# Performance work log

Measured on AMD Instinct MI355X. Metric: run time of the kernel, lower is better.

## Reference

```python
import jax, jax.numpy as jnp
import numpy as np

N = 50000      # num nodes
E = 800000     # num edges (avg degree 16)
F_IN = 64      # num_node_features
D = 64         # layer_hidden_dim (= out_channels per layer)
H = 8          # num_heads
C = D // H     # head_dim = 8
L = 5          # num_gnn_layers


def setup_inputs() -> dict:
    key = jax.random.key(0)
    ks = jax.random.split(key, 8)
    x = jax.random.normal(ks[0], (N, F_IN), jnp.float32)
    edge_index = jax.random.randint(ks[1], (2, E), 0, N, dtype=jnp.int32)
    # input embedding Linear(F_IN, D): weight stored as [in, out]
    W_in = jax.random.normal(ks[2], (F_IN, D), jnp.float32) * 0.1
    b_in = jnp.zeros((D,), jnp.float32)
    # per-layer GAT params, stacked over L layers
    lin_w = jax.random.normal(ks[3], (L, D, D), jnp.float32) * 0.1
    lin_b = jnp.zeros((L, D), jnp.float32)
    att = jax.random.normal(ks[4], (L, H, 2 * C), jnp.float32) * 0.1
    out_bias = jnp.zeros((L, D), jnp.float32)
    ln_g = jnp.ones((L, D), jnp.float32)
    ln_b = jnp.zeros((L, D), jnp.float32)
    return {"x": x, "edge_index": edge_index, "W_in": W_in, "b_in": b_in,
            "lin_w": lin_w, "lin_b": lin_b, "att": att, "out_bias": out_bias,
            "ln_g": ln_g, "ln_b": ln_b}


def _gat_layer(h, src, dst, Wl, bl, al, ob, g, b):
    # h: [N, D] -> per-head features [N, H, C]
    hp = (h @ Wl + bl).reshape(N, H, C)
    xi = hp[dst]          # [E, H, C] target-node features (x_i)
    xj = hp[src]          # [E, H, C] source-node features (x_j)
    # cat([x_i, x_j]) . att  == x_i . att[:, :C] + x_j . att[:, C:]
    alpha = jnp.einsum('ehc,hc->eh', xi, al[:, :C]) + \
            jnp.einsum('ehc,hc->eh', xj, al[:, C:])          # [E, H]
    alpha = jax.nn.leaky_relu(alpha, negative_slope=0.2)
    # segment softmax over target index (numerically stable)
    m = jax.ops.segment_max(alpha, dst, num_segments=N)      # [N, H]
    ea = jnp.exp(alpha - m[dst])
    s = jax.ops.segment_sum(ea, dst, num_segments=N)         # [N, H]
    w = ea / (s[dst] + 1e-16)                                # [E, H]
    # message = x_j * alpha, aggr='add'
    agg = jax.ops.segment_sum(xj * w[:, :, None], dst, num_segments=N)  # [N, H, C]
    out = agg.reshape(N, H * C) + ob
    out = jax.nn.elu(out)
    # LayerNorm over feature dim (eval mode: dropout = identity)
    mu = out.mean(-1, keepdims=True)
    var = out.var(-1, keepdims=True)
    return (out - mu) * jax.lax.rsqrt(var + 1e-5) * g + b


def reference(x, edge_index, W_in, b_in, lin_w, lin_b, att, out_bias, ln_g, ln_b):
    src = edge_index[0]
    dst = edge_index[1]   # PyG source_to_target: index = edge_index[1]
    h = jax.nn.relu(x @ W_in + b_in)
    for l in range(L):
        h = _gat_layer(h, src, dst, lin_w[l], lin_b[l], att[l],
                       out_bias[l], ln_g[l], ln_b[l])
    return h
```

## Files before the change

### kernel.cpp

```cpp
#include <hip/hip_runtime.h>
#include <hip/hip_bf16.h>

#define DD 64
#define LL 5
#define KPAD 64
#define L2E 1.4426950408889634f

typedef __attribute__((ext_vector_type(8))) short short8;
typedef __attribute__((ext_vector_type(4))) float float4v;

__device__ __forceinline__ short f2bf_bits(float f) {
    __hip_bfloat16 h = __float2bfloat16(f);
    return *reinterpret_cast<short*>(&h);
}
__device__ __forceinline__ float bfbits2f(short s) {
    __hip_bfloat16 h = *reinterpret_cast<__hip_bfloat16*>(&s);
    return __bfloat162float(h);
}

__device__ __forceinline__ int sniffw(const unsigned short* xb) {
    int lane = threadIdx.x & 63;
    int e = (xb[lane * 2] >> 7) & 0xFF;
    return __any(e >= 134) ? 1 : 0;
}

__global__ void allcvt_k(const void* __restrict__ x, const void* __restrict__ W_in,
                         const void* __restrict__ b_in, const void* __restrict__ lw,
                         const void* __restrict__ lb, const void* __restrict__ att,
                         const void* __restrict__ ob, const void* __restrict__ lg,
                         const void* __restrict__ lbb,
                         unsigned short* __restrict__ xhi, unsigned short* __restrict__ xlo,
                         float* __restrict__ wts,
                         unsigned short* __restrict__ whiT, unsigned short* __restrict__ wloT,
                         int* __restrict__ deg,
                         int nelem, int nxb, int n) {
    int bid = blockIdx.x;
    int fl = sniffw((const unsigned short*)x);
    if (bid < nxb) {
        int i = bid * 256 + threadIdx.x;
        if (i < nelem) {
            float v = fl ? ((const float*)x)[i] : (float)((const __hip_bfloat16*)x)[i];
            short hi = f2bf_bits(v);
            xhi[i] = (unsigned short)hi;
            xlo[i] = (unsigned short)f2bf_bits(v - bfbits2f(hi));
        }
    } else if (bid < nxb + 104) {
        int i = (bid - nxb) * 256 + threadIdx.x;
        if (i >= 26560) return;
        const void* p; int o;
        if      (i < 4096)  { p = W_in; o = i; }
        else if (i < 4160)  { p = b_in; o = i - 4096; }
        else if (i < 24640) { p = lw;   o = i - 4160; }
        else if (i < 24960) { p = lb;   o = i - 24640; }
        else if (i < 25600) { p = att;  o = i - 24960; }
        else if (i < 25920) { p = ob;   o = i - 25600; }
        else if (i < 26240) { p = lg;   o = i - 25920; }
        else                { p = lbb;  o = i - 26240; }
        wts[i] = fl ? ((const float*)p)[o] : (float)((const __hip_bfloat16*)p)[o];
    } else if (bid < nxb + 104 + 96) {
        int i = (bid - nxb - 104) * 256 + threadIdx.x;
        if (i >= 6 * 4096) return;
        const void* p; int o;
        if (i < 4096) { p = W_in; o = i; } else { p = lw; o = i - 4096; }
        float v = fl ? ((const float*)p)[o] : (float)((const __hip_bfloat16*)p)[o];
        short hi = f2bf_bits(v);
        short lo = f2bf_bits(v - bfbits2f(hi));
        int mat = i >> 12, rem = i & 4095, k = rem >> 6, col = rem & 63;
        int t = mat * 4096 + col * 64 + k;
        whiT[t] = (unsigned short)hi;
        wloT[t] = (unsigned short)lo;
    } else {
        int i = (bid - nxb - 104 - 96) * 256 + threadIdx.x;
        if (i < n) deg[i] = 0;
    }
}

__global__ void csrpad_k(const int* __restrict__ src, const int* __restrict__ dst,
                         int* __restrict__ deg, unsigned short* __restrict__ csr_pad,
                         int e, int psize, int n) {
    int p = blockIdx.x & 7;
    int chunk = blockIdx.x >> 3;
    int lo = p * psize;
    int hi = min(lo + psize, n);
    int base = chunk * 2048 + threadIdx.x;
#pragma unroll
    for (int k = 0; k < 8; ++k) {
        int i = base + k * 256;
        if (i < e) {
            int d = dst[i];
            if (d >= lo && d < hi) {
                int slot = atomicAdd(&deg[d], 1);
                if (slot < KPAD) csr_pad[d * KPAD + slot] = (unsigned short)src[i];
            }
        }
    }
}

__device__ __forceinline__ void gemm_from_lds(
        const unsigned short (*AH)[72], const unsigned short (*AL)[72],
        const unsigned short* __restrict__ Whi, const unsigned short* __restrict__ Wlo,
        const float* __restrict__ bias, const float* __restrict__ Att,
        unsigned short* __restrict__ hp_out, float* __restrict__ bd,
        float* __restrict__ ss, int base, int n) {
    int lane = threadIdx.x & 63;
    int wave = threadIdx.x >> 6;
    int m = lane & 15;
    int q = lane >> 4;
    int coln = wave * 16 + m;

    short8 ah0 = *reinterpret_cast<const short8*>(&AH[m][q * 8]);
    short8 ah1 = *reinterpret_cast<const short8*>(&AH[m][32 + q * 8]);
    short8 al0 = *reinterpret_cast<const short8*>(&AL[m][q * 8]);
    short8 al1 = *reinterpret_cast<const short8*>(&AL[m][32 + q * 8]);

    short8 bh0 = *reinterpret_cast<const short8*>(Whi + coln * 64 + q * 8);
    short8 bh1 = *reinterpret_cast<const short8*>(Whi + coln * 64 + 32 + q * 8);
    short8 bl0 = *reinterpret_cast<const short8*>(Wlo + coln * 64 + q * 8);
    short8 bl1 = *reinterpret_cast<const short8*>(Wlo + coln * 64 + 32 + q * 8);

    float4v acc = {0.f, 0.f, 0.f, 0.f};
    acc = __builtin_amdgcn_mfma_f32_16x16x32_bf16(ah0, bh0, acc, 0, 0, 0);
    acc = __builtin_amdgcn_mfma_f32_16x16x32_bf16(al0, bh0, acc, 0, 0, 0);
    acc = __builtin_amdgcn_mfma_f32_16x16x32_bf16(ah0, bl0, acc, 0, 0, 0);
    acc = __builtin_amdgcn_mfma_f32_16x16x32_bf16(ah1, bh1, acc, 0, 0, 0);
    acc = __builtin_amdgcn_mfma_f32_16x16x32_bf16(al1, bh1, acc, 0, 0, 0);
    acc = __builtin_amdgcn_mfma_f32_16x16x32_bf16(ah1, bl1, acc, 0, 0, 0);

    float bc = bias[coln];
    int c_ = m & 7;
    int hh = 2 * wave + (m >> 3);
    float attd = Att[hh * 16 + c_];
    float atts = Att[hh * 16 + 8 + c_];
#pragma unroll
    for (int r = 0; r < 4; ++r) {
        int rr = base + q * 4 + r;
        float v = acc[r] + bc;
        short vb = f2bf_bits(v);
        float vr = bfbits2f(vb);
        if (rr < n) hp_out[(size_t)rr * 64 + coln] = (unsigned short)vb;
        float bdv = vr * attd;
        float ssv = vr * atts;
        bdv += __shfl_xor(bdv, 1, 64);
        bdv += __shfl_xor(bdv, 2, 64);
        bdv += __shfl_xor(bdv, 4, 64);
        ssv += __shfl_xor(ssv, 1, 64);
        ssv += __shfl_xor(ssv, 2, 64);
        ssv += __shfl_xor(ssv, 4, 64);
        if ((m & 7) == 0 && rr < n) {
            bd[rr * 8 + hh] = bdv * L2E;
            ss[rr * 8 + hh] = ssv * L2E;
        }
    }
}

__global__ void __launch_bounds__(256) k0_k(const unsigned short* __restrict__ xhi,
                                            const unsigned short* __restrict__ xlo,
                                            const unsigned short* __restrict__ whiT,
                                            const unsigned short* __restrict__ wloT,
                                            const float* __restrict__ bias_in,
                                            const float* __restrict__ bias_l0,
                                            const float* __restrict__ att0,
                                            unsigned short* __restrict__ hp_out,
                                            float* __restrict__ bd, float* __restrict__ ss,
                                            int n) {
    __shared__ unsigned short AH[16][72];
    __shared__ unsigned short AL[16][72];
    int lane = threadIdx.x & 63;
    int wave = threadIdx.x >> 6;
    int m = lane & 15;
    int q = lane >> 4;
    int coln = wave * 16 + m;
    int base = blockIdx.x * 16;

    {
        int arow = min(base + m, n - 1);
        const unsigned short* ap = xhi + (size_t)arow * 64 + q * 8;
        const unsigned short* alp = xlo + (size_t)arow * 64 + q * 8;
        short8 ah0 = *reinterpret_cast<const short8*>(ap);
        short8 ah1 = *reinterpret_cast<const short8*>(ap + 32);
        short8 al0 = *reinterpret_cast<const short8*>(alp);
        short8 al1 = *reinterpret_cast<const short8*>(alp + 32);
        short8 bh0 = *reinterpret_cast<const short8*>(whiT + coln * 64 + q * 8);
        short8 bh1 = *reinterpret_cast<const short8*>(whiT + coln * 64 + 32 + q * 8);
        short8 bl0 = *reinterpret_cast<const short8*>(wloT + coln * 64 + q * 8);
        short8 bl1 = *reinterpret_cast<const short8*>(wloT + coln * 64 + 32 + q * 8);
        float4v acc = {0.f, 0.f, 0.f, 0.f};
        acc = __builtin_amdgcn_mfma_f32_16x16x32_bf16(ah0, bh0, acc, 0, 0, 0);
        acc = __builtin_amdgcn_mfma_f32_16x16x32_bf16(al0, bh0, acc, 0, 0, 0);
        acc = __builtin_amdgcn_mfma_f32_16x16x32_bf16(ah0, bl0, acc, 0, 0, 0);
        acc = __builtin_amdgcn_mfma_f32_16x16x32_bf16(ah1, bh1, acc, 0, 0, 0);
        acc = __builtin_amdgcn_mfma_f32_16x16x32_bf16(al1, bh1, acc, 0, 0, 0);
        acc = __builtin_amdgcn_mfma_f32_16x16x32_bf16(ah1, bl1, acc, 0, 0, 0);
        float bc = bias_in[coln];
#pragma unroll
        for (int r = 0; r < 4; ++r) {
            float v = fmaxf(acc[r] + bc, 0.f);
            short hi = f2bf_bits(v);
            AH[q * 4 + r][coln] = (unsigned short)hi;
            AL[q * 4 + r][coln] = (unsigned short)f2bf_bits(v - bfbits2f(hi));
        }
    }
    __syncthreads();
    gemm_from_lds(AH, AL, whiT + 4096, wloT + 4096, bias_l0, att0,
                  hp_out, bd, ss, base, n);
}

__global__ void __launch_bounds__(256) layer_k(const unsigned short* __restrict__ hpbf,
                                               const int* __restrict__ deg,
                                               const unsigned short* __restrict__ csr,
                                               const float* __restrict__ bd_in,
                                               const float* __restrict__ ss_in,
                                               const float* __restrict__ ob,
                                               const float* __restrict__ g,
                                               const float* __restrict__ b,
                                               const unsigned short* __restrict__ Wnhi,
                                               const unsigned short* __restrict__ Wnlo,
                                               const float* __restrict__ bias_n,
                                               const float* __restrict__ att_n,
                                               unsigned short* __restrict__ hp_out,
                                               float* __restrict__ bd_out,
                                               float* __restrict__ ss_out,
                                               void* __restrict__ outp,
                                               const unsigned short* __restrict__ xb,
                                               int n, int last) {
    __shared__ unsigned short AH[16][72];
    __shared__ unsigned short AL[16][72];
    int lane = threadIdx.x & 63;
    int wave = threadIdx.x >> 6;
    int base = blockIdx.x * 16;

    int h1 = lane & 7;
    int e1 = lane >> 3;
    int qt = lane >> 4;
    int fq = lane & 15;
    int h2 = fq >> 1;
    int bb = qt * 32 + h2 * 4;

    int fl = last ? sniffw(xb) : 0;

    float r0 = 0.f, r1 = 0.f, r2 = 0.f, r3 = 0.f, rsum = 0.f;

    for (int nd = 0; nd < 4; ++nd) {
        int node = base + wave * 4 + nd;
        if (node < n) {
            int node_u = __builtin_amdgcn_readfirstlane(node);
            float bh1 = bd_in[node_u * 8 + h1];
            int dd = __builtin_amdgcn_readfirstlane(min(deg[node_u], KPAD));
            int nchunk = (dd + 7) >> 3;
            const unsigned short* csrn = csr + node_u * KPAD;
            const unsigned* csrd = (const unsigned*)csrn;

            float s_acc = 0.f;
            float a0 = 0.f, a1 = 0.f, a2 = 0.f, a3 = 0.f;

            int c = 0;
            for (; c + 2 <= nchunk; c += 2) {
                int slotA = c * 8 + e1;
                int slotB = slotA + 8;
                int jA1 = csrn[slotA];
                float aA = bh1 + ss_in[jA1 * 8 + h1];
                aA = (aA > 0.f) ? aA : 0.2f * aA;
                float wA = exp2f(fminf(aA, 60.f));
                float wB = 0.f;
                if (slotB < dd) {
                    int jB1 = csrn[slotB];
                    float aB = bh1 + ss_in[jB1 * 8 + h1];
                    aB = (aB > 0.f) ? aB : 0.2f * aB;
                    wB = exp2f(fminf(aB, 60.f));
                }
                s_acc += wA + wB;
                unsigned sA0 = csrd[c * 4 + 0];
                unsigned sA1 = csrd[c * 4 + 1];
                unsigned sA2 = csrd[c * 4 + 2];
                unsigned sA3 = csrd[c * 4 + 3];
                unsigned sB0 = csrd[c * 4 + 4];
                unsigned sB1 = csrd[c * 4 + 5];
                unsigned sB2 = csrd[c * 4 + 6];
                unsigned sB3 = csrd[c * 4 + 7];
#pragma unroll
                for (int p = 0; p < 2; ++p) {
                    {
                        unsigned dwlo = p ? sA2 : sA0;
                        unsigned dwhi = p ? sA3 : sA1;
                        unsigned dw = (qt & 2) ? dwhi : dwlo;
                        int j = (qt & 1) ? (int)(dw >> 16) : (int)(dw & 0xffffu);
                        j = min(j, n - 1);
                        float we = __int_as_float(
                            __builtin_amdgcn_ds_bpermute(bb + 128 * p, __float_as_int(wA)));
                        uint2 d2 = *reinterpret_cast<const uint2*>(hpbf + (size_t)j * 64 + fq * 4);
                        a0 = fmaf(__int_as_float((int)(d2.x << 16)), we, a0);
                        a1 = fmaf(__int_as_float((int)(d2.x & 0xffff0000u)), we, a1);
                        a2 = fmaf(__int_as_float((int)(d2.y << 16)), we, a2);
                        a3 = fmaf(__int_as_float((int)(d2.y & 0xffff0000u)), we, a3);
                    }
                    {
                        unsigned dwlo = p ? sB2 : sB0;
                        unsigned dwhi = p ? sB3 : sB1;
                        unsigned dw = (qt & 2) ? dwhi : dwlo;
                        int j = (qt & 1) ? (int)(dw >> 16) : (int)(dw & 0xffffu);
                        j = min(j, n - 1);
                        float we = __int_as_float(
                            __builtin_amdgcn_ds_bpermute(bb + 128 * p, __float_as_int(wB)));
                        uint2 d2 = *reinterpret_cast<const uint2*>(hpbf + (size_t)j * 64 + fq * 4);
                        a0 = fmaf(__int_as_float((int)(d2.x << 16)), we, a0);
                        a1 = fmaf(__int_as_float((int)(d2.x & 0xffff0000u)), we, a1);
                        a2 = fmaf(__int_as_float((int)(d2.y << 16)), we, a2);
                        a3 = fmaf(__int_as_float((int)(d2.y & 0xffff0000u)), we, a3);
                    }
                }
            }
            if (c < nchunk) {
                int slot = c * 8 + e1;
                float w = 0.f;
                if (slot < dd) {
                    int j1 = csrn[slot];
                    float a = bh1 + ss_in[j1 * 8 + h1];
                    a = (a > 0.f) ? a : 0.2f * a;
                    w = exp2f(fminf(a, 60.f));
                }
                s_acc += w;
                unsigned s0 = csrd[c * 4 + 0];
                unsigned s1 = csrd[c * 4 + 1];
                unsigned s2 = csrd[c * 4 + 2];
                unsigned s3 = csrd[c * 4 + 3];
#pragma unroll
                for (int p = 0; p < 2; ++p) {
                    unsigned dwlo = p ? s2 : s0;
                    unsigned dwhi = p ? s3 : s1;
                    unsigned dw = (qt & 2) ? dwhi : dwlo;
                    int j = (qt & 1) ? (int)(dw >> 16) : (int)(dw & 0xffffu);
                    j = min(j, n - 1);
                    float we = __int_as_float(
                        __builtin_amdgcn_ds_bpermute(bb + 128 * p, __float_as_int(w)));
                    uint2 d2 = *reinterpret_cast<const uint2*>(hpbf + (size_t)j * 64 + fq * 4);
                    a0 = fmaf(__int_as_float((int)(d2.x << 16)), we, a0);
                    a1 = fmaf(__int_as_float((int)(d2.x & 0xffff0000u)), we, a1);
                    a2 = fmaf(__int_as_float((int)(d2.y << 16)), we, a2);
                    a3 = fmaf(__int_as_float((int)(d2.y & 0xffff0000u)), we, a3);
                }
            }

            float ssum = s_acc;
            ssum += __shfl_xor(ssum, 8, 64);
            ssum += __shfl_xor(ssum, 16, 64);
            ssum += __shfl_xor(ssum, 32, 64);

            a0 += __shfl_xor(a0, 16, 64); a0 += __shfl_xor(a0, 32, 64);
            a1 += __shfl_xor(a1, 16, 64); a1 += __shfl_xor(a1, 32, 64);
            a2 += __shfl_xor(a2, 16, 64); a2 += __shfl_xor(a2, 32, 64);
            a3 += __shfl_xor(a3, 16, 64); a3 += __shfl_xor(a3, 32, 64);

            if (qt == nd) { r0 = a0; r1 = a1; r2 = a2; r3 = a3; rsum = ssum; }
        }
    }

    float sh = __int_as_float(
        __builtin_amdgcn_ds_bpermute((qt * 16 + h2) * 4, __float_as_int(rsum)));
    float rinv = __builtin_amdgcn_rcpf(sh + 1e-16f);
    float4 ob4 = ((const float4*)ob)[fq];
    float o0 = r0 * rinv + ob4.x;
    float o1 = r1 * rinv + ob4.y;
    float o2 = r2 * rinv + ob4.z;
    float o3 = r3 * rinv + ob4.w;
    o0 = (o0 > 0.f) ? o0 : exp2f(o0 * L2E) - 1.f;
    o1 = (o1 > 0.f) ? o1 : exp2f(o1 * L2E) - 1.f;
    o2 = (o2 > 0.f) ? o2 : exp2f(o2 * L2E) - 1.f;
    o3 = (o3 > 0.f) ? o3 : exp2f(o3 * L2E) - 1.f;

    float ps = o0 + o1 + o2 + o3;
#pragma unroll
    for (int d = 1; d < 16; d <<= 1) ps += __shfl_xor(ps, d, 64);
    float mu = ps * (1.f / 64.f);
    float d0 = o0 - mu, d1 = o1 - mu, d2v = o2 - mu, d3 = o3 - mu;
    float sq = d0 * d0 + d1 * d1 + d2v * d2v + d3 * d3;
#pragma unroll
    for (int d = 1; d < 16; d <<= 1) sq += __shfl_xor(sq, d, 64);
    float rstd = __builtin_amdgcn_rsqf(sq * (1.f / 64.f) + 1e-5f);
    float4 g4 = ((const float4*)g)[fq];
    float4 b4 = ((const float4*)b)[fq];
    float y0 = d0 * rstd * g4.x + b4.x;
    float y1 = d1 * rstd * g4.y + b4.y;
    float y2 = d2v * rstd * g4.z + b4.z;
    float y3 = d3 * rstd * g4.w + b4.w;

    int onode = base + wave * 4 + qt;
    if (!last) {
        int ridx = wave * 4 + qt;
        short hb0 = f2bf_bits(y0), hb1 = f2bf_bits(y1);
        short hb2 = f2bf_bits(y2), hb3 = f2bf_bits(y3);
        unsigned hA = (unsigned short)hb0 | ((unsigned)(unsigned short)hb1 << 16);
        unsigned hB = (unsigned short)hb2 | ((unsigned)(unsigned short)hb3 << 16);
        uint2 yh = {hA, hB};
        unsigned lA = (unsigned short)f2bf_bits(y0 - bfbits2f(hb0)) |
                      ((unsigned)(unsigned short)f2bf_bits(y1 - bfbits2f(hb1)) << 16);
        unsigned lB = (unsigned short)f2bf_bits(y2 - bfbits2f(hb2)) |
                      ((unsigned)(unsigned short)f2bf_bits(y3 - bfbits2f(hb3)) << 16);
        uint2 yl = {lA, lB};
        *reinterpret_cast<uint2*>(&AH[ridx][fq * 4]) = yh;
        *reinterpret_cast<uint2*>(&AL[ridx][fq * 4]) = yl;
    } else if (onode < n) {
        if (fl) {
            float4 y = {y0, y1, y2, y3};
            ((float4*)outp)[(size_t)onode * 16 + fq] = y;
        } else {
            unsigned lo = (unsigned short)f2bf_bits(y0) |
                          ((unsigned)(unsigned short)f2bf_bits(y1) << 16);
            unsigned hi = (unsigned short)f2bf_bits(y2) |
                          ((unsigned)(unsigned short)f2bf_bits(y3) << 16);
            uint2 y = {lo, hi};
            ((uint2*)outp)[(size_t)onode * 16 + fq] = y;
        }
    }

    if (last) return;
    __syncthreads();
    gemm_from_lds(AH, AL, Wnhi, Wnlo, bias_n, att_n, hp_out, bd_out, ss_out, base, n);
}

static void* g_pool = nullptr;
static size_t g_pool_sz = 0;

extern "C" void kernel_launch(void* const* d_in, const int* in_sizes, int n_in,
                              void* d_out, int out_size, void* d_ws, size_t ws_size,
                              hipStream_t stream) {
    const void* x    = d_in[0];
    const int* ei    = (const int*)d_in[1];
    const void* W_in = d_in[2];
    const void* b_in = d_in[3];
    const void* lw   = d_in[4];
    const void* lb   = d_in[5];
    const void* att  = d_in[6];
    const void* ob   = d_in[7];
    const void* lg   = d_in[8];
    const void* lbb  = d_in[9];

    const int n = in_sizes[0] / DD;
    const int e = in_sizes[1] / 2;
    const int* src = ei;
    const int* dst = ei + e;

    auto align256 = [](size_t v) { return (v + 255) & ~(size_t)255; };
    size_t need = 0;
    size_t off_xhi  = need; need += align256((size_t)n * DD * 2);
    size_t off_xlo  = need; need += align256((size_t)n * DD * 2);
    size_t off_hpA  = need; need += align256((size_t)n * DD * 2);
    size_t off_hpB  = need; need += align256((size_t)n * DD * 2);
    size_t off_deg  = need; need += align256((size_t)n * 4);
    size_t off_csr  = need; need += align256((size_t)n * KPAD * 2);
    size_t off_wts  = need; need += align256((size_t)26560 * 4);
    size_t off_bdA  = need; need += align256((size_t)n * 8 * 4);
    size_t off_ssA  = need; need += align256((size_t)n * 8 * 4);
    size_t off_bdB  = need; need += align256((size_t)n * 8 * 4);
    size_t off_ssB  = need; need += align256((size_t)n * 8 * 4);
    size_t off_whi  = need; need += align256((size_t)6 * 4096 * 2);
    size_t off_wlo  = need; need += align256((size_t)6 * 4096 * 2);

    char* ws;
    if (ws_size >= need) {
        ws = (char*)d_ws;
    } else {
        if (g_pool == nullptr || g_pool_sz < need) {
            hipMalloc(&g_pool, need);
            g_pool_sz = need;
        }
        ws = (char*)g_pool;
    }

    unsigned short* xhi = (unsigned short*)(ws + off_xhi);
    unsigned short* xlo = (unsigned short*)(ws + off_xlo);
    unsigned short* hpA = (unsigned short*)(ws + off_hpA);
    unsigned short* hpB = (unsigned short*)(ws + off_hpB);
    int* deg     = (int*)(ws + off_deg);
    unsigned short* csr = (unsigned short*)(ws + off_csr);
    float* wts   = (float*)(ws + off_wts);
    float* bdA   = (float*)(ws + off_bdA);
    float* ssA   = (float*)(ws + off_ssA);
    float* bdB   = (float*)(ws + off_bdB);
    float* ssB   = (float*)(ws + off_ssB);
    unsigned short* whiT = (unsigned short*)(ws + off_whi);
    unsigned short* wloT = (unsigned short*)(ws + off_wlo);

    float* wb_in = wts + 4096;
    float* wlb   = wts + 24640;
    float* watt  = wts + 24960;
    float* wob   = wts + 25600;
    float* wlg   = wts + 25920;
    float* wlbb  = wts + 26240;

    int nelem = n * DD;
    int nxb = (nelem + 255) / 256;
    int degb = (n + 255) / 256;
    allcvt_k<<<nxb + 104 + 96 + degb, 256, 0, stream>>>(
        x, W_in, b_in, lw, lb, att, ob, lg, lbb,
        xhi, xlo, wts, whiT, wloT, deg, nelem, nxb, n);

    int psize = (n + 7) / 8;
    int chunks = (e + 2047) / 2048;
    csrpad_k<<<chunks * 8, 256, 0, stream>>>(src, dst, deg, csr, e, psize, n);

    int nb16 = (n + 15) / 16;
    k0_k<<<nb16, 256, 0, stream>>>(xhi, xlo, whiT, wloT, wb_in, wlb, watt,
                                   hpA, bdA, ssA, n);

    for (int l = 0; l < LL; ++l) {
        int last = (l == LL - 1) ? 1 : 0;
        unsigned short* hin = (l & 1) ? hpB : hpA;
        float* bdi = (l & 1) ? bdB : bdA;
        float* ssi = (l & 1) ? ssB : ssA;
        unsigned short* hout = (l & 1) ? hpA : hpB;
        float* bdo = (l & 1) ? bdA : bdB;
        float* sso = (l & 1) ? ssA : ssB;
        layer_k<<<nb16, 256, 0, stream>>>(
            hin, deg, csr, bdi, ssi,
            wob + (size_t)l * DD, wlg + (size_t)l * DD, wlbb + (size_t)l * DD,
            whiT + (size_t)(l + 2) * 4096, wloT + (size_t)(l + 2) * 4096,
            wlb + (size_t)(l + 1) * DD, watt + (size_t)(l + 1) * 128,
            hout, bdo, sso, d_out, (const unsigned short*)x, n, last);
    }
}
```

Measured before the change: 318.7 us.

## Process four nodes per wave concurrently with software-pipelined gathers, 32-row blocks

The per-layer aggregation used to walk a wave's nodes one at a time. It now handles four nodes together in gat_quad, with loads issued ahead of compute in unrolled stages chosen by the maximum chunk count, to raise memory-level parallelism on the neighbor gathers. Each block now covers 32 nodes (8 per wave, in two passes), and the fused next-layer GEMM runs on 32 rows with a new gemm_from_lds32. Buffers are padded so the int4 degree loads and clamped indices stay in range. The cost is higher register pressure, hinted with launch_bounds(256,6), and wasted lanes when the four nodes' degrees differ.

```diff
diff --git a/kernel.cpp b/kernel.cpp
--- a/kernel.cpp
+++ b/kernel.cpp
@@ -16,6 +16,9 @@
 __device__ __forceinline__ float bfbits2f(short s) {
     __hip_bfloat16 h = *reinterpret_cast<__hip_bfloat16*>(&s);
     return __bfloat162float(h);
+}
+__device__ __forceinline__ float bperm(int addr, float v) {
+    return __int_as_float(__builtin_amdgcn_ds_bpermute(addr, __float_as_int(v)));
 }
 
 __device__ __forceinline__ int sniffw(const unsigned short* xb) {
@@ -153,6 +156,67 @@
     }
 }
 
+__device__ __forceinline__ void gemm_from_lds32(
+        const unsigned short (*AH)[72], const unsigned short (*AL)[72],
+        const unsigned short* __restrict__ Whi, const unsigned short* __restrict__ Wlo,
+        const float* __restrict__ bias, const float* __restrict__ Att,
+        unsigned short* __restrict__ hp_out, float* __restrict__ bd,
+        float* __restrict__ ss, int base, int n) {
+    int lane = threadIdx.x & 63;
+    int wave = threadIdx.x >> 6;
+    int m = lane & 15;
+    int q = lane >> 4;
+    int coln = wave * 16 + m;
+
+    short8 bh0 = *reinterpret_cast<const short8*>(Whi + coln * 64 + q * 8);
+    short8 bh1 = *reinterpret_cast<const short8*>(Whi + coln * 64 + 32 + q * 8);
+    short8 bl0 = *reinterpret_cast<const short8*>(Wlo + coln * 64 + q * 8);
+    short8 bl1 = *reinterpret_cast<const short8*>(Wlo + coln * 64 + 32 + q * 8);
+
+    float bc = bias[coln];
+    int c_ = m & 7;
+    int hh = 2 * wave + (m >> 3);
+    float attd = Att[hh * 16 + c_];
+    float atts = Att[hh * 16 + 8 + c_];
+
+#pragma unroll
+    for (int mi = 0; mi < 2; ++mi) {
+        short8 ah0 = *reinterpret_cast<const short8*>(&AH[mi * 16 + m][q * 8]);
+        short8 ah1 = *reinterpret_cast<const short8*>(&AH[mi * 16 + m][32 + q * 8]);
+        short8 al0 = *reinterpret_cast<const short8*>(&AL[mi * 16 + m][q * 8]);
+        short8 al1 = *reinterpret_cast<const short8*>(&AL[mi * 16 + m][32 + q * 8]);
+
+        float4v acc = {0.f, 0.f, 0.f, 0.f};
+        acc = __builtin_amdgcn_mfma_f32_16x16x32_bf16(ah0, bh0, acc, 0, 0, 0);
+        acc = __builtin_amdgcn_mfma_f32_16x16x32_bf16(al0, bh0, acc, 0, 0, 0);
+        acc = __builtin_amdgcn_mfma_f32_16x16x32_bf16(ah0, bl0, acc, 0, 0, 0);
+        acc = __builtin_amdgcn_mfma_f32_16x16x32_bf16(ah1, bh1, acc, 0, 0, 0);
+        acc = __builtin_amdgcn_mfma_f32_16x16x32_bf16(al1, bh1, acc, 0, 0, 0);
+        acc = __builtin_amdgcn_mfma_f32_16x16x32_bf16(ah1, bl1, acc, 0, 0, 0);
+
+#pragma unroll
+        for (int r = 0; r < 4; ++r) {
+            int rr = base + mi * 16 + q * 4 + r;
+            float v = acc[r] + bc;
+            short vb = f2bf_bits(v);
+            float vr = bfbits2f(vb);
+            if (rr < n) hp_out[(size_t)rr * 64 + coln] = (unsigned short)vb;
+            float bdv = vr * attd;
+            float ssv = vr * atts;
+            bdv += __shfl_xor(bdv, 1, 64);
+            bdv += __shfl_xor(bdv, 2, 64);
+            bdv += __shfl_xor(bdv, 4, 64);
+            ssv += __shfl_xor(ssv, 1, 64);
+            ssv += __shfl_xor(ssv, 2, 64);
+            ssv += __shfl_xor(ssv, 4, 64);
+            if ((m & 7) == 0 && rr < n) {
+                bd[rr * 8 + hh] = bdv * L2E;
+                ss[rr * 8 + hh] = ssv * L2E;
+            }
+        }
+    }
+}
+
 __global__ void __launch_bounds__(256) k0_k(const unsigned short* __restrict__ xhi,
                                             const unsigned short* __restrict__ xlo,
                                             const unsigned short* __restrict__ whiT,
@@ -205,7 +269,151 @@
                   hp_out, bd, ss, base, n);
 }
 
-__global__ void __launch_bounds__(256) layer_k(const unsigned short* __restrict__ hpbf,
+#define EXJ(W, j) { unsigned ws_ = (e1 & 4) ? ((e1 & 2) ? W.w : W.z) : ((e1 & 2) ? W.y : W.x); \
+    j = (e1 & 1) ? (int)(ws_ >> 16) : (int)(ws_ & 0xffffu); j = min(j, nm1); }
+#define EXG(W, g0, g1) { unsigned d0_ = (qt & 2) ? W.y : W.x; unsigned d1_ = (qt & 2) ? W.w : W.z; \
+    g0 = (qt & 1) ? (int)(d0_ >> 16) : (int)(d0_ & 0xffffu); \
+    g1 = (qt & 1) ? (int)(d1_ >> 16) : (int)(d1_ & 0xffffu); \
+    g0 = min(g0, nm1); g1 = min(g1, nm1); }
+#define FMA4(V, W, A0, A1, A2, A3) \
+    A0 = fmaf(__int_as_float((int)(V.x << 16)), W, A0); \
+    A1 = fmaf(__int_as_float((int)(V.x & 0xffff0000u)), W, A1); \
+    A2 = fmaf(__int_as_float((int)(V.y << 16)), W, A2); \
+    A3 = fmaf(__int_as_float((int)(V.y & 0xffff0000u)), W, A3);
+
+#define QDECL(ST) uint2 ST##v00, ST##v01, ST##v10, ST##v11, ST##v20, ST##v21, ST##v30, ST##v31; \
+    float ST##ss0, ST##ss1, ST##ss2, ST##ss3;
+
+#define QLOAD(ST, ci) { \
+    uint4 w0_ = c0[ci]; uint4 w1_ = c1[ci]; uint4 w2_ = c2[ci]; uint4 w3_ = c3[ci]; \
+    { int j_; EXJ(w0_, j_) ST##ss0 = ss_in[j_ * 8 + h1]; } \
+    { int j_; EXJ(w1_, j_) ST##ss1 = ss_in[j_ * 8 + h1]; } \
+    { int j_; EXJ(w2_, j_) ST##ss2 = ss_in[j_ * 8 + h1]; } \
+    { int j_; EXJ(w3_, j_) ST##ss3 = ss_in[j_ * 8 + h1]; } \
+    { int g0_, g1_; EXG(w0_, g0_, g1_) \
+      ST##v00 = *reinterpret_cast<const uint2*>(hpbf + (size_t)g0_ * 64 + fq4); \
+      ST##v01 = *reinterpret_cast<const uint2*>(hpbf + (size_t)g1_ * 64 + fq4); } \
+    { int g0_, g1_; EXG(w1_, g0_, g1_) \
+      ST##v10 = *reinterpret_cast<const uint2*>(hpbf + (size_t)g0_ * 64 + fq4); \
+      ST##v11 = *reinterpret_cast<const uint2*>(hpbf + (size_t)g1_ * 64 + fq4); } \
+    { int g0_, g1_; EXG(w2_, g0_, g1_) \
+      ST##v20 = *reinterpret_cast<const uint2*>(hpbf + (size_t)g0_ * 64 + fq4); \
+      ST##v21 = *reinterpret_cast<const uint2*>(hpbf + (size_t)g1_ * 64 + fq4); } \
+    { int g0_, g1_; EXG(w3_, g0_, g1_) \
+      ST##v30 = *reinterpret_cast<const uint2*>(hpbf + (size_t)g0_ * 64 + fq4); \
+      ST##v31 = *reinterpret_cast<const uint2*>(hpbf + (size_t)g1_ * 64 + fq4); } \
+}
+
+#define QCOMP(ST, ci) { \
+    int slot_ = (ci) * 8 + e1; \
+    { float aa_ = bh0 + ST##ss0; aa_ = (aa_ > 0.f) ? aa_ : 0.2f * aa_; \
+      float wg_ = (slot_ < dd0) ? exp2f(fminf(aa_, 60.f)) : 0.f; \
+      s0 += wg_; \
+      float wp0_ = bperm(bb, wg_); float wp1_ = bperm(bb + 128, wg_); \
+      FMA4(ST##v00, wp0_, a00, a01, a02, a03) \
+      FMA4(ST##v01, wp1_, a00, a01, a02, a03) } \
+    { float aa_ = bh1v + ST##ss1; aa_ = (aa_ > 0.f) ? aa_ : 0.2f * aa_; \
+      float wg_ = (slot_ < dd1) ? exp2f(fminf(aa_, 60.f)) : 0.f; \
+      s1 += wg_; \
+      float wp0_ = bperm(bb, wg_); float wp1_ = bperm(bb + 128, wg_); \
+      FMA4(ST##v10, wp0_, a10, a11, a12, a13) \
+      FMA4(ST##v11, wp1_, a10, a11, a12, a13) } \
+    { float aa_ = bh2v + ST##ss2; aa_ = (aa_ > 0.f) ? aa_ : 0.2f * aa_; \
+      float wg_ = (slot_ < dd2) ? exp2f(fminf(aa_, 60.f)) : 0.f; \
+      s2 += wg_; \
+      float wp0_ = bperm(bb, wg_); float wp1_ = bperm(bb + 128, wg_); \
+      FMA4(ST##v20, wp0_, a20, a21, a22, a23) \
+      FMA4(ST##v21, wp1_, a20, a21, a22, a23) } \
+    { float aa_ = bh3v + ST##ss3; aa_ = (aa_ > 0.f) ? aa_ : 0.2f * aa_; \
+      float wg_ = (slot_ < dd3) ? exp2f(fminf(aa_, 60.f)) : 0.f; \
+      s3 += wg_; \
+      float wp0_ = bperm(bb, wg_); float wp1_ = bperm(bb + 128, wg_); \
+      FMA4(ST##v30, wp0_, a30, a31, a32, a33) \
+      FMA4(ST##v31, wp1_, a30, a31, a32, a33) } \
+}
+
+__device__ __forceinline__ void gat_quad(
+        const unsigned short* __restrict__ hpbf,
+        const float* __restrict__ ss_in,
+        const unsigned short* __restrict__ csr,
+        int u0, int u1, int u2, int u3,
+        int dd0, int dd1, int dd2, int dd3,
+        float bh0, float bh1v, float bh2v, float bh3v,
+        int e1, int h1, int qt, int fq4, int bb, int nm1,
+        float& r0, float& r1, float& r2, float& r3, float& rsum) {
+    const uint4* c0 = reinterpret_cast<const uint4*>(csr + (size_t)u0 * KPAD);
+    const uint4* c1 = reinterpret_cast<const uint4*>(csr + (size_t)u1 * KPAD);
+    const uint4* c2 = reinterpret_cast<const uint4*>(csr + (size_t)u2 * KPAD);
+    const uint4* c3 = reinterpret_cast<const uint4*>(csr + (size_t)u3 * KPAD);
+    int ncm = (max(max(dd0, dd1), max(dd2, dd3)) + 7) >> 3;
+
+    float s0 = 0.f, s1 = 0.f, s2 = 0.f, s3 = 0.f;
+    float a00 = 0.f, a01 = 0.f, a02 = 0.f, a03 = 0.f;
+    float a10 = 0.f, a11 = 0.f, a12 = 0.f, a13 = 0.f;
+    float a20 = 0.f, a21 = 0.f, a22 = 0.f, a23 = 0.f;
+    float a30 = 0.f, a31 = 0.f, a32 = 0.f, a33 = 0.f;
+
+    if (ncm <= 2) {
+        QDECL(P) QDECL(Q)
+        QLOAD(P, 0)
+        QLOAD(Q, 1)
+        QCOMP(P, 0)
+        QCOMP(Q, 1)
+    } else if (ncm == 3) {
+        QDECL(P) QDECL(Q) QDECL(R)
+        QLOAD(P, 0)
+        QLOAD(Q, 1)
+        QCOMP(P, 0)
+        QLOAD(R, 2)
+        QCOMP(Q, 1)
+        QCOMP(R, 2)
+    } else if (ncm == 4) {
+        QDECL(P) QDECL(Q) QDECL(R) QDECL(S)
+        QLOAD(P, 0)
+        QLOAD(Q, 1)
+        QCOMP(P, 0)
+        QLOAD(R, 2)
+        QCOMP(Q, 1)
+        QLOAD(S, 3)
+        QCOMP(R, 2)
+        QCOMP(S, 3)
+    } else {
+        for (int c = 0; c < ncm; ++c) {
+            QDECL(T)
+            QLOAD(T, c)
+            QCOMP(T, c)
+        }
+    }
+
+    s0 += __shfl_xor(s0, 8, 64); s0 += __shfl_xor(s0, 16, 64); s0 += __shfl_xor(s0, 32, 64);
+    s1 += __shfl_xor(s1, 8, 64); s1 += __shfl_xor(s1, 16, 64); s1 += __shfl_xor(s1, 32, 64);
+    s2 += __shfl_xor(s2, 8, 64); s2 += __shfl_xor(s2, 16, 64); s2 += __shfl_xor(s2, 32, 64);
+    s3 += __shfl_xor(s3, 8, 64); s3 += __shfl_xor(s3, 16, 64); s3 += __shfl_xor(s3, 32, 64);
+
+    a00 += __shfl_xor(a00, 16, 64); a00 += __shfl_xor(a00, 32, 64);
+    a01 += __shfl_xor(a01, 16, 64); a01 += __shfl_xor(a01, 32, 64);
+    a02 += __shfl_xor(a02, 16, 64); a02 += __shfl_xor(a02, 32, 64);
+    a03 += __shfl_xor(a03, 16, 64); a03 += __shfl_xor(a03, 32, 64);
+    a10 += __shfl_xor(a10, 16, 64); a10 += __shfl_xor(a10, 32, 64);
+    a11 += __shfl_xor(a11, 16, 64); a11 += __shfl_xor(a11, 32, 64);
+    a12 += __shfl_xor(a12, 16, 64); a12 += __shfl_xor(a12, 32, 64);
+    a13 += __shfl_xor(a13, 16, 64); a13 += __shfl_xor(a13, 32, 64);
+    a20 += __shfl_xor(a20, 16, 64); a20 += __shfl_xor(a20, 32, 64);
+    a21 += __shfl_xor(a21, 16, 64); a21 += __shfl_xor(a21, 32, 64);
+    a22 += __shfl_xor(a22, 16, 64); a22 += __shfl_xor(a22, 32, 64);
+    a23 += __shfl_xor(a23, 16, 64); a23 += __shfl_xor(a23, 32, 64);
+    a30 += __shfl_xor(a30, 16, 64); a30 += __shfl_xor(a30, 32, 64);
+    a31 += __shfl_xor(a31, 16, 64); a31 += __shfl_xor(a31, 32, 64);
+    a32 += __shfl_xor(a32, 16, 64); a32 += __shfl_xor(a32, 32, 64);
+    a33 += __shfl_xor(a33, 16, 64); a33 += __shfl_xor(a33, 32, 64);
+
+    if (qt == 0) { r0 = a00; r1 = a01; r2 = a02; r3 = a03; rsum = s0; }
+    if (qt == 1) { r0 = a10; r1 = a11; r2 = a12; r3 = a13; rsum = s1; }
+    if (qt == 2) { r0 = a20; r1 = a21; r2 = a22; r3 = a23; rsum = s2; }
+    if (qt == 3) { r0 = a30; r1 = a31; r2 = a32; r3 = a33; rsum = s3; }
+}
+
+__global__ void __launch_bounds__(256, 6) layer_k(const unsigned short* __restrict__ hpbf,
                                                const int* __restrict__ deg,
                                                const unsigned short* __restrict__ csr,
                                                const float* __restrict__ bd_in,
@@ -223,198 +431,107 @@
                                                void* __restrict__ outp,
                                                const unsigned short* __restrict__ xb,
                                                int n, int last) {
-    __shared__ unsigned short AH[16][72];
-    __shared__ unsigned short AL[16][72];
+    __shared__ unsigned short AH[32][72];
+    __shared__ unsigned short AL[32][72];
     int lane = threadIdx.x & 63;
     int wave = threadIdx.x >> 6;
-    int base = blockIdx.x * 16;
+    int base = blockIdx.x * 32;
 
     int h1 = lane & 7;
     int e1 = lane >> 3;
     int qt = lane >> 4;
     int fq = lane & 15;
+    int fq4 = fq * 4;
     int h2 = fq >> 1;
     int bb = qt * 32 + h2 * 4;
+    int nm1 = n - 1;
 
     int fl = last ? sniffw(xb) : 0;
-
-    float r0 = 0.f, r1 = 0.f, r2 = 0.f, r3 = 0.f, rsum = 0.f;
-
-    for (int nd = 0; nd < 4; ++nd) {
-        int node = base + wave * 4 + nd;
-        if (node < n) {
-            int node_u = __builtin_amdgcn_readfirstlane(node);
-            float bh1 = bd_in[node_u * 8 + h1];
-            int dd = __builtin_amdgcn_readfirstlane(min(deg[node_u], KPAD));
-            int nchunk = (dd + 7) >> 3;
-            const unsigned short* csrn = csr + node_u * KPAD;
-            const unsigned* csrd = (const unsigned*)csrn;
-
-            float s_acc = 0.f;
-            float a0 = 0.f, a1 = 0.f, a2 = 0.f, a3 = 0.f;
-
-            int c = 0;
-            for (; c + 2 <= nchunk; c += 2) {
-                int slotA = c * 8 + e1;
-                int slotB = slotA + 8;
-                int jA1 = csrn[slotA];
-                float aA = bh1 + ss_in[jA1 * 8 + h1];
-                aA = (aA > 0.f) ? aA : 0.2f * aA;
-                float wA = exp2f(fminf(aA, 60.f));
-                float wB = 0.f;
-                if (slotB < dd) {
-                    int jB1 = csrn[slotB];
-                    float aB = bh1 + ss_in[jB1 * 8 + h1];
-                    aB = (aB > 0.f) ? aB : 0.2f * aB;
-                    wB = exp2f(fminf(aB, 60.f));
-                }
-                s_acc += wA + wB;
-                unsigned sA0 = csrd[c * 4 + 0];
-                unsigned sA1 = csrd[c * 4 + 1];
-                unsigned sA2 = csrd[c * 4 + 2];
-                unsigned sA3 = csrd[c * 4 + 3];
-                unsigned sB0 = csrd[c * 4 + 4];
-                unsigned sB1 = csrd[c * 4 + 5];
-                unsigned sB2 = csrd[c * 4 + 6];
-                unsigned sB3 = csrd[c * 4 + 7];
+    int nd0 = base + wave * 8;
+
+#pragma unroll 1
+    for (int pass = 0; pass < 2; ++pass) {
+        int np = nd0 + pass * 4;
+        int4 dv = *reinterpret_cast<const int4*>(deg + np);
+        int dd0 = __builtin_amdgcn_readfirstlane((np + 0 < n) ? min(dv.x, KPAD) : 0);
+        int dd1 = __builtin_amdgcn_readfirstlane((np + 1 < n) ? min(dv.y, KPAD) : 0);
+        int dd2 = __builtin_amdgcn_readfirstlane((np + 2 < n) ? min(dv.z, KPAD) : 0);
+        int dd3 = __builtin_amdgcn_readfirstlane((np + 3 < n) ? min(dv.w, KPAD) : 0);
+        float bh0 = bd_in[min(np + 0, nm1) * 8 + h1];
+        float bh1v = bd_in[min(np + 1, nm1) * 8 + h1];
+        float bh2v = bd_in[min(np + 2, nm1) * 8 + h1];
+        float bh3v = bd_in[min(np + 3, nm1) * 8 + h1];
+        int u0 = __builtin_amdgcn_readfirstlane(min(np + 0, nm1));
+        int u1 = __builtin_amdgcn_readfirstlane(min(np + 1, nm1));
+        int u2 = __builtin_amdgcn_readfirstlane(min(np + 2, nm1));
+        int u3 = __builtin_amdgcn_readfirstlane(min(np + 3, nm1));
+
+        float r0 = 0.f, r1 = 0.f, r2 = 0.f, r3 = 0.f, rsum = 0.f;
+        gat_quad(hpbf, ss_in, csr, u0, u1, u2, u3, dd0, dd1, dd2, dd3,
+                 bh0, bh1v, bh2v, bh3v, e1, h1, qt, fq4, bb, nm1,
+                 r0, r1, r2, r3, rsum);
+
+        float sh = bperm((qt * 16 + h2) * 4, rsum);
+        float rinv = __builtin_amdgcn_rcpf(sh + 1e-16f);
+        float4 ob4 = ((const float4*)ob)[fq];
+        float o0 = r0 * rinv + ob4.x;
+        float o1 = r1 * rinv + ob4.y;
+        float o2 = r2 * rinv + ob4.z;
+        float o3 = r3 * rinv + ob4.w;
+        o0 = (o0 > 0.f) ? o0 : exp2f(o0 * L2E) - 1.f;
+        o1 = (o1 > 0.f) ? o1 : exp2f(o1 * L2E) - 1.f;
+        o2 = (o2 > 0.f) ? o2 : exp2f(o2 * L2E) - 1.f;
+        o3 = (o3 > 0.f) ? o3 : exp2f(o3 * L2E) - 1.f;
+
+        float ps = o0 + o1 + o2 + o3;
 #pragma unroll
-                for (int p = 0; p < 2; ++p) {
-                    {
-                        unsigned dwlo = p ? sA2 : sA0;
-                        unsigned dwhi = p ? sA3 : sA1;
-                        unsigned dw = (qt & 2) ? dwhi : dwlo;
-                        int j = (qt & 1) ? (int)(dw >> 16) : (int)(dw & 0xffffu);
-                        j = min(j, n - 1);
-                        float we = __int_as_float(
-                            __builtin_amdgcn_ds_bpermute(bb + 128 * p, __float_as_int(wA)));
-                        uint2 d2 = *reinterpret_cast<const uint2*>(hpbf + (size_t)j * 64 + fq * 4);
-                        a0 = fmaf(__int_as_float((int)(d2.x << 16)), we, a0);
-                        a1 = fmaf(__int_as_float((int)(d2.x & 0xffff0000u)), we, a1);
-                        a2 = fmaf(__int_as_float((int)(d2.y << 16)), we, a2);
-                        a3 = fmaf(__int_as_float((int)(d2.y & 0xffff0000u)), we, a3);
-                    }
-                    {
-                        unsigned dwlo = p ? sB2 : sB0;
-                        unsigned dwhi = p ? sB3 : sB1;
-                        unsigned dw = (qt & 2) ? dwhi : dwlo;
-                        int j = (qt & 1) ? (int)(dw >> 16) : (int)(dw & 0xffffu);
-                        j = min(j, n - 1);
-                        float we = __int_as_float(
-                            __builtin_amdgcn_ds_bpermute(bb + 128 * p, __float_as_int(wB)));
-                        uint2 d2 = *reinterpret_cast<const uint2*>(hpbf + (size_t)j * 64 + fq * 4);
-                        a0 = fmaf(__int_as_float((int)(d2.x << 16)), we, a0);
-                        a1 = fmaf(__int_as_float((int)(d2.x & 0xffff0000u)), we, a1);
-                        a2 = fmaf(__int_as_float((int)(d2.y << 16)), we, a2);
-                        a3 = fmaf(__int_as_float((int)(d2.y & 0xffff0000u)), we, a3);
-                    }
-                }
+        for (int d = 1; d < 16; d <<= 1) ps += __shfl_xor(ps, d, 64);
+        float mu = ps * (1.f / 64.f);
+        float d0 = o0 - mu, d1 = o1 - mu, d2v = o2 - mu, d3 = o3 - mu;
+        float sq = d0 * d0 + d1 * d1 + d2v * d2v + d3 * d3;
+#pragma unroll
+        for (int d = 1; d < 16; d <<= 1) sq += __shfl_xor(sq, d, 64);
+        float rstd = __builtin_amdgcn_rsqf(sq * (1.f / 64.f) + 1e-5f);
+        float4 g4 = ((const float4*)g)[fq];
+        float4 b4 = ((const float4*)b)[fq];
+        float y0 = d0 * rstd * g4.x + b4.x;
+        float y1 = d1 * rstd * g4.y + b4.y;
+        float y2 = d2v * rstd * g4.z + b4.z;
+        float y3 = d3 * rstd * g4.w + b4.w;
+
+        int onode = np + qt;
+        if (!last) {
+            int ridx = wave * 8 + pass * 4 + qt;
+            short hb0 = f2bf_bits(y0), hb1 = f2bf_bits(y1);
+            short hb2 = f2bf_bits(y2), hb3 = f2bf_bits(y3);
+            unsigned hA = (unsigned short)hb0 | ((unsigned)(unsigned short)hb1 << 16);
+            unsigned hB = (unsigned short)hb2 | ((unsigned)(unsigned short)hb3 << 16);
+            uint2 yh = {hA, hB};
+            unsigned lA = (unsigned short)f2bf_bits(y0 - bfbits2f(hb0)) |
+                          ((unsigned)(unsigned short)f2bf_bits(y1 - bfbits2f(hb1)) << 16);
+            unsigned lB = (unsigned short)f2bf_bits(y2 - bfbits2f(hb2)) |
+                          ((unsigned)(unsigned short)f2bf_bits(y3 - bfbits2f(hb3)) << 16);
+            uint2 yl = {lA, lB};
+            *reinterpret_cast<uint2*>(&AH[ridx][fq * 4]) = yh;
+            *reinterpret_cast<uint2*>(&AL[ridx][fq * 4]) = yl;
+        } else if (onode < n) {
+            if (fl) {
+                float4 y = {y0, y1, y2, y3};
+                ((float4*)outp)[(size_t)onode * 16 + fq] = y;
+            } else {
+                unsigned lo = (unsigned short)f2bf_bits(y0) |
+                              ((unsigned)(unsigned short)f2bf_bits(y1) << 16);
+                unsigned hi = (unsigned short)f2bf_bits(y2) |
+                              ((unsigned)(unsigned short)f2bf_bits(y3) << 16);
+                uint2 y = {lo, hi};
+                ((uint2*)outp)[(size_t)onode * 16 + fq] = y;
             }
-            if (c < nchunk) {
-                int slot = c * 8 + e1;
-                float w = 0.f;
-                if (slot < dd) {
-                    int j1 = csrn[slot];
-                    float a = bh1 + ss_in[j1 * 8 + h1];
-                    a = (a > 0.f) ? a : 0.2f * a;
-                    w = exp2f(fminf(a, 60.f));
-                }
-                s_acc += w;
-                unsigned s0 = csrd[c * 4 + 0];
-                unsigned s1 = csrd[c * 4 + 1];
-                unsigned s2 = csrd[c * 4 + 2];
-                unsigned s3 = csrd[c * 4 + 3];
-#pragma unroll
-                for (int p = 0; p < 2; ++p) {
-                    unsigned dwlo = p ? s2 : s0;
-                    unsigned dwhi = p ? s3 : s1;
-                    unsigned dw = (qt & 2) ? dwhi : dwlo;
-                    int j = (qt & 1) ? (int)(dw >> 16) : (int)(dw & 0xffffu);
-                    j = min(j, n - 1);
-                    float we = __int_as_float(
-                        __builtin_amdgcn_ds_bpermute(bb + 128 * p, __float_as_int(w)));
-                    uint2 d2 = *reinterpret_cast<const uint2*>(hpbf + (size_t)j * 64 + fq * 4);
-                    a0 = fmaf(__int_as_float((int)(d2.x << 16)), we, a0);
-                    a1 = fmaf(__int_as_float((int)(d2.x & 0xffff0000u)), we, a1);
-                    a2 = fmaf(__int_as_float((int)(d2.y << 16)), we, a2);
-                    a3 = fmaf(__int_as_float((int)(d2.y & 0xffff0000u)), we, a3);
-                }
-            }
-
-            float ssum = s_acc;
-            ssum += __shfl_xor(ssum, 8, 64);
-            ssum += __shfl_xor(ssum, 16, 64);
-            ssum += __shfl_xor(ssum, 32, 64);
-
-            a0 += __shfl_xor(a0, 16, 64); a0 += __shfl_xor(a0, 32, 64);
-            a1 += __shfl_xor(a1, 16, 64); a1 += __shfl_xor(a1, 32, 64);
-            a2 += __shfl_xor(a2, 16, 64); a2 += __shfl_xor(a2, 32, 64);
-            a3 += __shfl_xor(a3, 16, 64); a3 += __shfl_xor(a3, 32, 64);
-
-            if (qt == nd) { r0 = a0; r1 = a1; r2 = a2; r3 = a3; rsum = ssum; }
-        }
-    }
-
-    float sh = __int_as_float(
-        __builtin_amdgcn_ds_bpermute((qt * 16 + h2) * 4, __float_as_int(rsum)));
-    float rinv = __builtin_amdgcn_rcpf(sh + 1e-16f);
-    float4 ob4 = ((const float4*)ob)[fq];
-    float o0 = r0 * rinv + ob4.x;
-    float o1 = r1 * rinv + ob4.y;
-    float o2 = r2 * rinv + ob4.z;
-    float o3 = r3 * rinv + ob4.w;
-    o0 = (o0 > 0.f) ? o0 : exp2f(o0 * L2E) - 1.f;
-    o1 = (o1 > 0.f) ? o1 : exp2f(o1 * L2E) - 1.f;
-    o2 = (o2 > 0.f) ? o2 : exp2f(o2 * L2E) - 1.f;
-    o3 = (o3 > 0.f) ? o3 : exp2f(o3 * L2E) - 1.f;
-
-    float ps = o0 + o1 + o2 + o3;
-#pragma unroll
-    for (int d = 1; d < 16; d <<= 1) ps += __shfl_xor(ps, d, 64);
-    float mu = ps * (1.f / 64.f);
-    float d0 = o0 - mu, d1 = o1 - mu, d2v = o2 - mu, d3 = o3 - mu;
-    float sq = d0 * d0 + d1 * d1 + d2v * d2v + d3 * d3;
-#pragma unroll
-    for (int d = 1; d < 16; d <<= 1) sq += __shfl_xor(sq, d, 64);
-    float rstd = __builtin_amdgcn_rsqf(sq * (1.f / 64.f) + 1e-5f);
-    float4 g4 = ((const float4*)g)[fq];
-    float4 b4 = ((const float4*)b)[fq];
-    float y0 = d0 * rstd * g4.x + b4.x;
-    float y1 = d1 * rstd * g4.y + b4.y;
-    float y2 = d2v * rstd * g4.z + b4.z;
-    float y3 = d3 * rstd * g4.w + b4.w;
-
-    int onode = base + wave * 4 + qt;
-    if (!last) {
-        int ridx = wave * 4 + qt;
-        short hb0 = f2bf_bits(y0), hb1 = f2bf_bits(y1);
-        short hb2 = f2bf_bits(y2), hb3 = f2bf_bits(y3);
-        unsigned hA = (unsigned short)hb0 | ((unsigned)(unsigned short)hb1 << 16);
-        unsigned hB = (unsigned short)hb2 | ((unsigned)(unsigned short)hb3 << 16);
-        uint2 yh = {hA, hB};
-        unsigned lA = (unsigned short)f2bf_bits(y0 - bfbits2f(hb0)) |
-                      ((unsigned)(unsigned short)f2bf_bits(y1 - bfbits2f(hb1)) << 16);
-        unsigned lB = (unsigned short)f2bf_bits(y2 - bfbits2f(hb2)) |
-                      ((unsigned)(unsigned short)f2bf_bits(y3 - bfbits2f(hb3)) << 16);
-        uint2 yl = {lA, lB};
-        *reinterpret_cast<uint2*>(&AH[ridx][fq * 4]) = yh;
-        *reinterpret_cast<uint2*>(&AL[ridx][fq * 4]) = yl;
-    } else if (onode < n) {
-        if (fl) {
-            float4 y = {y0, y1, y2, y3};
-            ((float4*)outp)[(size_t)onode * 16 + fq] = y;
-        } else {
-            unsigned lo = (unsigned short)f2bf_bits(y0) |
-                          ((unsigned)(unsigned short)f2bf_bits(y1) << 16);
-            unsigned hi = (unsigned short)f2bf_bits(y2) |
-                          ((unsigned)(unsigned short)f2bf_bits(y3) << 16);
-            uint2 y = {lo, hi};
-            ((uint2*)outp)[(size_t)onode * 16 + fq] = y;
         }
     }
 
     if (last) return;
     __syncthreads();
-    gemm_from_lds(AH, AL, Wnhi, Wnlo, bias_n, att_n, hp_out, bd_out, ss_out, base, n);
+    gemm_from_lds32(AH, AL, Wnhi, Wnlo, bias_n, att_n, hp_out, bd_out, ss_out, base, n);
 }
 
 static void* g_pool = nullptr;
@@ -443,9 +560,9 @@
     size_t need = 0;
     size_t off_xhi  = need; need += align256((size_t)n * DD * 2);
     size_t off_xlo  = need; need += align256((size_t)n * DD * 2);
-    size_t off_hpA  = need; need += align256((size_t)n * DD * 2);
-    size_t off_hpB  = need; need += align256((size_t)n * DD * 2);
-    size_t off_deg  = need; need += align256((size_t)n * 4);
+    size_t off_hpA  = need; need += align256((size_t)(n + 32) * DD * 2);
+    size_t off_hpB  = need; need += align256((size_t)(n + 32) * DD * 2);
+    size_t off_deg  = need; need += align256((size_t)(n + 32) * 4);
     size_t off_csr  = need; need += align256((size_t)n * KPAD * 2);
     size_t off_wts  = need; need += align256((size_t)26560 * 4);
     size_t off_bdA  = need; need += align256((size_t)n * 8 * 4);
@@ -502,6 +619,7 @@
     k0_k<<<nb16, 256, 0, stream>>>(xhi, xlo, whiT, wloT, wb_in, wlb, watt,
                                    hpA, bdA, ssA, n);
 
+    int nb32 = (n + 31) / 32;
     for (int l = 0; l < LL; ++l) {
         int last = (l == LL - 1) ? 1 : 0;
         unsigned short* hin = (l & 1) ? hpB : hpA;
@@ -510,7 +628,7 @@
         unsigned short* hout = (l & 1) ? hpA : hpB;
         float* bdo = (l & 1) ? bdA : bdB;
         float* sso = (l & 1) ? ssA : ssB;
-        layer_k<<<nb16, 256, 0, stream>>>(
+        layer_k<<<nb32, 256, 0, stream>>>(
             hin, deg, csr, bdi, ssi,
             wob + (size_t)l * DD, wlg + (size_t)l * DD, wlbb + (size_t)l * DD,
             whiT + (size_t)(l + 2) * 4096, wloT + (size_t)(l + 2) * 4096,
```

New measurement: 672.1 us. 2.11x slower.
